# Kernel optimization log

Measured on AMD Instinct MI355X. Metric: run time of the kernel, lower is better.

## Reference

```python
import jax, jax.numpy as jnp
import numpy as np

N_BINS = 15


def setup_inputs() -> dict:
    key = jax.random.key(0)
    k1, k2 = jax.random.split(key)
    N, C = 2097152, 100
    logits = jax.random.normal(k1, (N, C), dtype=jnp.float32)
    labels = jax.random.randint(k2, (N,), 0, C, dtype=jnp.int64)
    return {"logits": logits, "labels": labels}


def reference(logits, labels):
    # softmax probabilities, top-1 confidence and prediction
    softmaxes = jax.nn.softmax(logits, axis=-1)          # [N, C]
    confidences = jnp.max(softmaxes, axis=1)             # [N]
    predictions = jnp.argmax(softmaxes, axis=1)          # [N]
    accuracies = (predictions == labels).astype(logits.dtype)

    n = logits.shape[0]
    # Torch bins are (i/n_bins, (i+1)/n_bins]; ceil(c*n_bins)-1 maps c into bin i.
    # confidences >= 1/C > 0, so every sample lands in some bin.
    bin_idx = jnp.clip(jnp.ceil(confidences * N_BINS).astype(jnp.int32) - 1, 0, N_BINS - 1)

    ones = jnp.ones_like(confidences)
    counts = jax.ops.segment_sum(ones, bin_idx, num_segments=N_BINS)         # [B]
    conf_sums = jax.ops.segment_sum(confidences, bin_idx, num_segments=N_BINS)
    acc_sums = jax.ops.segment_sum(accuracies, bin_idx, num_segments=N_BINS)

    prop_in_bin = counts / n
    safe_counts = jnp.maximum(counts, 1.0)
    gap = jnp.abs(conf_sums / safe_counts - acc_sums / safe_counts)
    ece = jnp.sum(jnp.where(counts > 0, gap * prop_in_bin, 0.0))
    return ece.reshape(1)
```

## Files before the change

### kernel.cpp

```cpp
#include <hip/hip_runtime.h>

typedef float f32x4 __attribute__((ext_vector_type(4)));

typedef __attribute__((address_space(1))) const void global_cv;
typedef __attribute__((address_space(3))) void lds_v;

#define N_BINS 15
#define NCLASS 100
#define ROWS   64
#define GRID   768

__global__ __launch_bounds__(256) void ece_pass1(
    const float* __restrict__ logits,
    const int* __restrict__ labels,
    float* __restrict__ bins,
    int n_rows, int niter)
{
    __shared__ __align__(16) float stage[2][ROWS * NCLASS];
    __shared__ float priv[45];

    const int tid  = threadIdx.x;
    const int wave = tid >> 6;
    const int q    = tid & 3;
    const int slot = tid >> 2;

    if (tid < 45) priv[tid] = 0.f;

    const long max_slot = (long)n_rows * (NCLASS / 4) - 1;
    const f32x4* gv = (const f32x4*)logits;

    auto issue_stage = [&](int buf, long row0) {
        if (row0 >= n_rows) return;
        const long s0 = row0 * (NCLASS / 4);
        #pragma unroll
        for (int r = 0; r < 6; ++r) {
            long si = s0 + r * 256 + tid;
            if (si > max_slot) si = max_slot;
            __builtin_amdgcn_global_load_lds(
                (global_cv*)(gv + si),
                (lds_v*)&stage[buf][(r * 256 + wave * 64) * 4],
                16, 0, 0);
        }
        if (wave == 0) {
            long si = s0 + 1536 + tid;
            if (si > max_slot) si = max_slot;
            __builtin_amdgcn_global_load_lds(
                (global_cv*)(gv + si),
                (lds_v*)&stage[buf][1536 * 4],
                16, 0, 0);
        }
    };

    issue_stage(0, (long)blockIdx.x * ROWS);

    for (int g = 0; g < niter; ++g) {
        __syncthreads();
        if (g + 1 < niter)
            issue_stage((g + 1) & 1,
                        ((long)(g + 1) * gridDim.x + blockIdx.x) * ROWS);

        const long row = ((long)g * gridDim.x + blockIdx.x) * ROWS + slot;
        const float* rp = &stage[g & 1][slot * NCLASS];
        const f32x4* rv = (const f32x4*)rp;

        int lab = 0;
        if (q == 0 && row < n_rows) lab = labels[row];

        f32x4 F[6];
        #pragma unroll
        for (int i = 0; i < 6; ++i) F[i] = rv[q + 4 * i];

        f32x4 T = { -1e30f, -1e30f, -1e30f, -1e30f };
        if (q == 0) T = rv[24];

        f32x4 m4 = F[0];
        f32x4 s4;
        s4.x = __expf(F[0].x); s4.y = __expf(F[0].y);
        s4.z = __expf(F[0].z); s4.w = __expf(F[0].w);
        #pragma unroll
        for (int i = 1; i < 6; ++i) {
            m4.x = fmaxf(m4.x, F[i].x); m4.y = fmaxf(m4.y, F[i].y);
            m4.z = fmaxf(m4.z, F[i].z); m4.w = fmaxf(m4.w, F[i].w);
            s4.x += __expf(F[i].x); s4.y += __expf(F[i].y);
            s4.z += __expf(F[i].z); s4.w += __expf(F[i].w);
        }
        m4.x = fmaxf(m4.x, T.x); m4.y = fmaxf(m4.y, T.y);
        m4.z = fmaxf(m4.z, T.z); m4.w = fmaxf(m4.w, T.w);
        s4.x += __expf(T.x); s4.y += __expf(T.y);
        s4.z += __expf(T.z); s4.w += __expf(T.w);

        float vm = fmaxf(fmaxf(m4.x, m4.y), fmaxf(m4.z, m4.w));
        float ss = (s4.x + s4.y) + (s4.z + s4.w);

        float pv = 0.f;
        if (q == 0) pv = rp[lab];

        #pragma unroll
        for (int off = 1; off <= 2; off <<= 1) {
            ss += __shfl_xor(ss, off, 4);
            vm = fmaxf(vm, __shfl_xor(vm, off, 4));
        }

        if (q == 0 && row < n_rows) {
            float conf = __expf(vm) / ss;
            int b = (int)ceilf(conf * (float)N_BINS) - 1;
            b = min(max(b, 0), N_BINS - 1);
            atomicAdd(&priv[b],      1.0f);
            atomicAdd(&priv[15 + b], conf);
            atomicAdd(&priv[30 + b], (pv == vm) ? 1.0f : 0.0f);
        }
    }

    __syncthreads();
    if (tid < 45) atomicAdd(&bins[tid], priv[tid]);
}

__global__ void ece_final(const float* __restrict__ bins,
                          float* __restrict__ out, float n)
{
    if (threadIdx.x == 0) {
        float ece = 0.f;
        for (int i = 0; i < N_BINS; ++i) {
            float cnt = bins[i];
            if (cnt > 0.f) {
                float sc  = fmaxf(cnt, 1.0f);
                float gap = fabsf(bins[15 + i] / sc - bins[30 + i] / sc);
                ece += gap * (cnt / n);
            }
        }
        out[0] = ece;
    }
}

extern "C" void kernel_launch(void* const* d_in, const int* in_sizes, int n_in,
                              void* d_out, int out_size, void* d_ws, size_t ws_size,
                              hipStream_t stream)
{
    const float* logits = (const float*)d_in[0];
    const int*   labels = (const int*)d_in[1];
    float* out  = (float*)d_out;
    float* bins = (float*)d_ws;

    const int n_rows = in_sizes[1];
    const int rows_per_sweep = GRID * ROWS;
    const int niter = (n_rows + rows_per_sweep - 1) / rows_per_sweep;

    hipMemsetAsync(bins, 0, 45 * sizeof(float), stream);
    ece_pass1<<<GRID, 256, 0, stream>>>(logits, labels, bins, n_rows, niter);
    ece_final<<<1, 64, 0, stream>>>(bins, out, (float)n_rows);
}
```

Before: 160.8 us.

## Stage labels via LDS, use per-wave vmcnt waits, fuse final reduction

Each wave now issues its own slice of the async global-to-LDS copies, labels included, and waits on vmcnt/lgkmcnt counters instead of a block-wide barrier before compute. The final ECE computation moves into the main kernel behind a last-block atomic counter, which removes the second launch. This is meant to cut barrier stalls, the scattered label loads and the launch overhead. It relies on hand-placed s_waitcnt counts matching the issued loads, and the barrier-free double buffering may let one wave overwrite a buffer that another wave is still reading.

```diff
diff --git a/kernel.cpp b/kernel.cpp
--- a/kernel.cpp
+++ b/kernel.cpp
@@ -14,57 +14,67 @@
     const float* __restrict__ logits,
     const int* __restrict__ labels,
     float* __restrict__ bins,
+    float* __restrict__ out,
     int n_rows, int niter)
 {
     __shared__ __align__(16) float stage[2][ROWS * NCLASS];
+    __shared__ int   lds_lab[2][ROWS];
     __shared__ float priv[45];
 
     const int tid  = threadIdx.x;
     const int wave = tid >> 6;
+    const int lane = tid & 63;
     const int q    = tid & 3;
     const int slot = tid >> 2;
 
     if (tid < 45) priv[tid] = 0.f;
+    __syncthreads();
 
     const long max_slot = (long)n_rows * (NCLASS / 4) - 1;
     const f32x4* gv = (const f32x4*)logits;
+    const int wbase = wave * 400;
 
-    auto issue_stage = [&](int buf, long row0) {
-        if (row0 >= n_rows) return;
-        const long s0 = row0 * (NCLASS / 4);
+    auto issue_stage = [&](int buf, int t) {
+        const long row0 = ((long)t * GRID + blockIdx.x) * ROWS;
+        const long s0   = row0 * (NCLASS / 4) + wbase;
         #pragma unroll
-        for (int r = 0; r < 6; ++r) {
-            long si = s0 + r * 256 + tid;
-            if (si > max_slot) si = max_slot;
+        for (int i = 0; i < 6; ++i) {
+            long si = s0 + i * 64 + lane;
+            si = (si > max_slot) ? max_slot : si;
             __builtin_amdgcn_global_load_lds(
                 (global_cv*)(gv + si),
-                (lds_v*)&stage[buf][(r * 256 + wave * 64) * 4],
-                16, 0, 0);
+                (lds_v*)&stage[buf][(wbase + i * 64) * 4], 16, 0, 0);
         }
-        if (wave == 0) {
-            long si = s0 + 1536 + tid;
-            if (si > max_slot) si = max_slot;
+        long si = s0 + 384 + lane;
+        si = (si > max_slot) ? max_slot : si;
+        long li = row0 + wave * 16 + lane;
+        li = (li > n_rows - 1) ? (n_rows - 1) : li;
+        if (lane < 16) {
             __builtin_amdgcn_global_load_lds(
                 (global_cv*)(gv + si),
-                (lds_v*)&stage[buf][1536 * 4],
-                16, 0, 0);
+                (lds_v*)&stage[buf][(wbase + 384) * 4], 16, 0, 0);
+            __builtin_amdgcn_global_load_lds(
+                (global_cv*)(labels + li),
+                (lds_v*)&lds_lab[buf][wave * 16], 4, 0, 0);
         }
     };
 
-    issue_stage(0, (long)blockIdx.x * ROWS);
+    issue_stage(0, 0);
 
-    for (int g = 0; g < niter; ++g) {
-        __syncthreads();
-        if (g + 1 < niter)
-            issue_stage((g + 1) & 1,
-                        ((long)(g + 1) * gridDim.x + blockIdx.x) * ROWS);
+    for (int t = 0; t < niter; ++t) {
+        asm volatile("s_waitcnt lgkmcnt(0)" ::: "memory");
+        if (t + 1 < niter) {
+            issue_stage((t + 1) & 1, t + 1);
+            asm volatile("s_waitcnt vmcnt(8)" ::: "memory");
+        } else {
+            asm volatile("s_waitcnt vmcnt(0)" ::: "memory");
+        }
+        __builtin_amdgcn_sched_barrier(0);
 
-        const long row = ((long)g * gridDim.x + blockIdx.x) * ROWS + slot;
-        const float* rp = &stage[g & 1][slot * NCLASS];
+        const long row = ((long)t * GRID + blockIdx.x) * ROWS + slot;
+        const float* rp = &stage[t & 1][slot * NCLASS];
         const f32x4* rv = (const f32x4*)rp;
-
-        int lab = 0;
-        if (q == 0 && row < n_rows) lab = labels[row];
+        const int lab = lds_lab[t & 1][slot];
 
         f32x4 F[6];
         #pragma unroll
@@ -113,22 +123,27 @@
 
     __syncthreads();
     if (tid < 45) atomicAdd(&bins[tid], priv[tid]);
-}
+    __threadfence();
+    __syncthreads();
 
-__global__ void ece_final(const float* __restrict__ bins,
-                          float* __restrict__ out, float n)
-{
-    if (threadIdx.x == 0) {
-        float ece = 0.f;
-        for (int i = 0; i < N_BINS; ++i) {
-            float cnt = bins[i];
-            if (cnt > 0.f) {
-                float sc  = fmaxf(cnt, 1.0f);
-                float gap = fabsf(bins[15 + i] / sc - bins[30 + i] / sc);
-                ece += gap * (cnt / n);
+    if (tid == 0) {
+        int* ctr = (int*)(bins + 45);
+        int old = atomicAdd(ctr, 1);
+        if (old == GRID - 1) {
+            const float n = (float)n_rows;
+            float ece = 0.f;
+            #pragma unroll
+            for (int i = 0; i < N_BINS; ++i) {
+                float cnt = atomicAdd(&bins[i], 0.0f);
+                if (cnt > 0.f) {
+                    float cs = atomicAdd(&bins[15 + i], 0.0f);
+                    float as = atomicAdd(&bins[30 + i], 0.0f);
+                    float sc = fmaxf(cnt, 1.0f);
+                    ece += fabsf(cs / sc - as / sc) * (cnt / n);
+                }
             }
+            out[0] = ece;
         }
-        out[0] = ece;
     }
 }
 
@@ -145,7 +160,6 @@
     const int rows_per_sweep = GRID * ROWS;
     const int niter = (n_rows + rows_per_sweep - 1) / rows_per_sweep;
 
-    hipMemsetAsync(bins, 0, 45 * sizeof(float), stream);
-    ece_pass1<<<GRID, 256, 0, stream>>>(logits, labels, bins, n_rows, niter);
-    ece_final<<<1, 64, 0, stream>>>(bins, out, (float)n_rows);
+    hipMemsetAsync(bins, 0, 48 * sizeof(float), stream);
+    ece_pass1<<<GRID, 256, 0, stream>>>(logits, labels, bins, out, n_rows, niter);
 }
```

Measured after the change: 271.8 us. 1.69x slower.
